# Optimization experiments

Hardware: AMD Instinct MI355X
Metric: run time of the kernel (lower is better)

Reference implementation:

```python
import jax, jax.numpy as jnp
import numpy as np

EOS_COEF = 0.1


def setup_inputs() -> dict:
    key = jax.random.key(0)
    k1, k2, k3, k4 = jax.random.split(key, 4)
    B, Q, T, P, M = 8, 256, 128, 100, 512
    pred_patch_logits = jax.random.normal(k1, (B, Q, 2), dtype=jnp.float32)
    pred_patch_points = jax.random.normal(k2, (B, Q, P, 3), dtype=jnp.float32)
    tgt_points = jax.random.normal(k3, (B, T, M, 3), dtype=jnp.float32)
    src_idx = jax.random.randint(k4, (B, T), 0, Q, dtype=jnp.int64)
    return {
        'pred_patch_logits': pred_patch_logits,
        'pred_patch_points': pred_patch_points,
        'tgt_points': tgt_points,
        'src_idx': src_idx,
    }


def reference(pred_patch_logits, pred_patch_points, tgt_points, src_idx):
    B, Q, C = pred_patch_logits.shape
    T = src_idx.shape[1]
    P = pred_patch_points.shape[2]
    M = tgt_points.shape[2]
    N = B * T  # total matched patches = num_patches
    bidx = jnp.arange(B)[:, None]

    # ---- loss_valid_labels (weighted CE, empty_weight = [1, eos_coef]) ----
    w = jnp.array([1.0, EOS_COEF], dtype=pred_patch_logits.dtype)
    target_classes = jnp.ones((B, Q), jnp.int32).at[bidx, src_idx].set(0)
    logp = jax.nn.log_softmax(pred_patch_logits, axis=-1)          # [B,Q,2]
    nll = -jnp.take_along_axis(logp, target_classes[..., None], axis=-1)[..., 0]
    wt = w[target_classes]
    loss_ce = jnp.sum(nll * wt) / jnp.sum(wt)

    # accuracy@1 on matched queries (targets are all class 0) and overall
    matched_logits = pred_patch_logits[bidx, src_idx]              # [B,T,2]
    acc_valid = 100.0 * jnp.mean((jnp.argmax(matched_logits, -1) == 0).astype(jnp.float32))
    acc_overall = 100.0 * jnp.mean((jnp.argmax(pred_patch_logits, -1) == target_classes).astype(jnp.float32))

    # ---- loss_cardinality (no-grad, logging) ----
    card_pred = jnp.sum((jnp.argmax(pred_patch_logits, -1) != (C - 1)).astype(jnp.float32), axis=1)
    card_err = jnp.mean(jnp.abs(card_pred - jnp.float32(T)))

    # ---- loss_geometry: per-patch squared chamfer, fused over all patches ----
    src = pred_patch_points[bidx, src_idx].reshape(N, P, 3)        # matched preds
    tgt = tgt_points.reshape(N, M, 3)
    # squared pairwise distances [N,P,M] = |a|^2 + |b|^2 - 2 a.b
    d2 = (jnp.sum(src * src, -1)[:, :, None]
          + jnp.sum(tgt * tgt, -1)[:, None, :]
          - 2.0 * jnp.einsum('npd,nmd->npm', src, tgt))
    d2 = jnp.maximum(d2, 0.0)
    per_patch = (jnp.mean(jnp.min(d2, axis=1), axis=-1)
                 + 0.2 * jnp.mean(jnp.min(d2, axis=2), axis=-1)) / 1.2  # [N]
    loss_geometry = jnp.sum(per_patch) / jnp.float32(N)

    return (loss_ce, acc_valid, acc_overall, card_err, loss_geometry)
```

## Files before the change

kernel.cpp:

```cpp
#include <hip/hip_runtime.h>
#include <math.h>

#define Bq 8
#define Qq 256
#define Tt 128
#define Pp 100
#define Mm 512
#define Nn 1024

__device__ __forceinline__ float breduce256(float v, float* red) {
    #pragma unroll
    for (int off = 32; off > 0; off >>= 1) v += __shfl_down(v, off, 64);
    __syncthreads();
    if ((threadIdx.x & 63) == 0) red[threadIdx.x >> 6] = v;
    __syncthreads();
    return red[0] + red[1] + red[2] + red[3];
}

__global__ __launch_bounds__(256) void geom_kernel(
    const float* __restrict__ pred_pts,
    const float* __restrict__ tgt_pts,
    const int*   __restrict__ src_idx,
    float*       __restrict__ per_patch)
{
    __shared__ float4   s_tgt[Mm];
    __shared__ float4   s_src[128];
    __shared__ unsigned s_amin[Mm];
    __shared__ float    s_bpart[8][128];
    __shared__ float    red[4];
    const int n   = blockIdx.x;
    const int tid = threadIdx.x;
    const int b   = n >> 7;
    const int q   = src_idx[n];
    const float* sp = pred_pts + (size_t)(b * Qq + q) * (Pp * 3);
    const float* tp = tgt_pts  + (size_t)n * (Mm * 3);

    {
        const float2* tp2 = (const float2*)tp;
        const float2 a = tp2[3*tid], c2 = tp2[3*tid+1], e = tp2[3*tid+2];
        s_tgt[2*tid]   = make_float4(a.x, a.y, c2.x, 0.f);
        s_tgt[2*tid+1] = make_float4(c2.y, e.x, e.y, 0.f);
    }
    if (tid < 50) {
        const float2* sp2 = (const float2*)sp;
        const float2 a = sp2[3*tid], c2 = sp2[3*tid+1], e = sp2[3*tid+2];
        s_src[2*tid]   = make_float4(a.x, a.y, c2.x, 0.f);
        s_src[2*tid+1] = make_float4(c2.y, e.x, e.y, 0.f);
    } else if (tid >= 100 && tid < 128) {
        s_src[tid] = make_float4(5e18f, 5e18f, 5e18f, 0.f);
    }
    *(uint2*)&s_amin[2*tid] = make_uint2(0x7f7fffffu, 0x7f7fffffu);
    __syncthreads();

    const int g = tid & 31;
    const int c = tid >> 5;
    const int mbase = c << 6;
    const float4 s0 = s_src[4*g+0], s1 = s_src[4*g+1],
                 s2 = s_src[4*g+2], s3 = s_src[4*g+3];
    float mn0 = 3.4e38f, mn1 = 3.4e38f, mn2 = 3.4e38f, mn3 = 3.4e38f;

    #pragma unroll 4
    for (int j = 0; j < 64; ++j) {
        const int m = mbase + ((j + g) & 63);
        const float4 t = s_tgt[m];
        float dx, dy, dz;
        dx = s0.x - t.x; dy = s0.y - t.y; dz = s0.z - t.z;
        const float d0 = fmaf(dx, dx, fmaf(dy, dy, dz * dz));
        dx = s1.x - t.x; dy = s1.y - t.y; dz = s1.z - t.z;
        const float d1 = fmaf(dx, dx, fmaf(dy, dy, dz * dz));
        dx = s2.x - t.x; dy = s2.y - t.y; dz = s2.z - t.z;
        const float d2 = fmaf(dx, dx, fmaf(dy, dy, dz * dz));
        dx = s3.x - t.x; dy = s3.y - t.y; dz = s3.z - t.z;
        const float d3 = fmaf(dx, dx, fmaf(dy, dy, dz * dz));
        mn0 = fminf(mn0, d0); mn1 = fminf(mn1, d1);
        mn2 = fminf(mn2, d2); mn3 = fminf(mn3, d3);
        const float pm = fminf(fminf(d0, d1), fminf(d2, d3));
        atomicMin(&s_amin[m], __float_as_uint(pm));
    }

    *(float4*)&s_bpart[c][4*g] = make_float4(mn0, mn1, mn2, mn3);
    __syncthreads();

    float contrib;
    {
        const uint2 u = *(const uint2*)&s_amin[2*tid];
        contrib = (__uint_as_float(u.x) + __uint_as_float(u.y)) * (1.0f / Mm);
    }
    if (tid < Pp) {
        float mn = s_bpart[0][tid];
        #pragma unroll
        for (int cc = 1; cc < 8; ++cc) mn = fminf(mn, s_bpart[cc][tid]);
        contrib += 0.2f * mn * (1.0f / Pp);
    }

    const float tot = breduce256(contrib, red);
    if (tid == 0) per_patch[n] = tot * (1.0f / 1.2f);
}

__global__ __launch_bounds__(256) void cls_kernel(
    const float* __restrict__ logits,
    const int*   __restrict__ src_idx,
    const float* __restrict__ per_patch,
    float*       __restrict__ out)
{
    __shared__ unsigned char matched[Bq * Qq];
    __shared__ int s_card[Bq];
    __shared__ float red[4];
    const int tid = threadIdx.x;
    for (int i = tid; i < Bq * Qq; i += 256) matched[i] = 0;
    if (tid < Bq) s_card[tid] = 0;
    __syncthreads();
    for (int i = tid; i < Nn; i += 256) {
        const int b = i >> 7;
        matched[b * Qq + src_idx[i]] = 1;
    }
    __syncthreads();

    float sum_nll = 0.f, sum_wt = 0.f, cnt_overall = 0.f;
    #pragma unroll
    for (int k = 0; k < (Bq * Qq) / 256; ++k) {
        const int i = tid + k * 256;
        const float l0 = logits[2*i], l1 = logits[2*i + 1];
        const int   mt = matched[i];
        const float mx  = fmaxf(l0, l1);
        const float lse = mx + logf(expf(l0 - mx) + expf(l1 - mx));
        const float lt  = mt ? l0 : l1;
        const float wt  = mt ? 1.0f : 0.1f;
        sum_nll += wt * (lse - lt);
        sum_wt  += wt;
        const int pred = (l0 >= l1) ? 0 : 1;
        const int c    = mt ? 0 : 1;
        cnt_overall += (pred == c) ? 1.f : 0.f;
        const unsigned long long bal = __ballot(pred == 0);
        if ((tid & 63) == 0) atomicAdd(&s_card[k], (int)__popcll(bal));
    }

    float cnt_valid = 0.f;
    for (int i = tid; i < Nn; i += 256) {
        const int b = i >> 7;
        const int q = src_idx[i];
        const float l0 = logits[2*(b*Qq + q)], l1 = logits[2*(b*Qq + q) + 1];
        cnt_valid += (l0 >= l1) ? 1.f : 0.f;
    }

    float gsum = 0.f;
    for (int i = tid; i < Nn; i += 256) gsum += per_patch[i];

    const float t_nll = breduce256(sum_nll,     red);
    const float t_wt  = breduce256(sum_wt,      red);
    const float t_ov  = breduce256(cnt_overall, red);
    const float t_va  = breduce256(cnt_valid,   red);
    const float t_gs  = breduce256(gsum,        red);
    __syncthreads();

    if (tid == 0) {
        float cerr = 0.f;
        for (int b = 0; b < Bq; ++b) cerr += fabsf((float)s_card[b] - (float)Tt);
        out[0] = t_nll / t_wt;
        out[1] = 100.f * t_va / (float)Nn;
        out[2] = 100.f * t_ov / (float)(Bq * Qq);
        out[3] = cerr / (float)Bq;
        out[4] = t_gs / (float)Nn;
    }
}

extern "C" void kernel_launch(void* const* d_in, const int* in_sizes, int n_in,
                              void* d_out, int out_size, void* d_ws, size_t ws_size,
                              hipStream_t stream) {
    const float* logits   = (const float*)d_in[0];
    const float* pred_pts = (const float*)d_in[1];
    const float* tgt_pts  = (const float*)d_in[2];
    const int*   src_idx  = (const int*)  d_in[3];
    float* out       = (float*)d_out;
    float* per_patch = (float*)d_ws;

    geom_kernel<<<Nn, 256, 0, stream>>>(pred_pts, tgt_pts, src_idx, per_patch);
    cls_kernel<<<1, 256, 0, stream>>>(logits, src_idx, per_patch, out);
}
```

Before: 86.73 us.

## Fuse classification into geometry kernel via last-block pattern and retile chamfer loop

Merges the single-block classification kernel into the geometry kernel. The last block to finish, found with an atomic done counter, computes the CE, accuracy, cardinality and final geometry sum, which removes a second launch but adds a memset per call. The chamfer inner loop is retiled so each thread holds 16 source points in registers against 16 targets, cutting target LDS reads and atomicMin count per distance. The target LDS layout is swizzled with an XOR to avoid bank conflicts. Per-source minima are now reduced with shared atomics instead of a partial array, and register pressure rises from holding 16 float4 plus 16 minima.

```diff
diff --git a/kernel.cpp b/kernel.cpp
--- a/kernel.cpp
+++ b/kernel.cpp
@@ -17,17 +17,21 @@
     return red[0] + red[1] + red[2] + red[3];
 }
 
-__global__ __launch_bounds__(256) void geom_kernel(
+__global__ __launch_bounds__(256) void fused_kernel(
+    const float* __restrict__ logits,
     const float* __restrict__ pred_pts,
     const float* __restrict__ tgt_pts,
     const int*   __restrict__ src_idx,
-    float*       __restrict__ per_patch)
+    float*       __restrict__ per_patch,
+    unsigned*    __restrict__ done_ctr,
+    float*       __restrict__ out)
 {
     __shared__ float4   s_tgt[Mm];
     __shared__ float4   s_src[128];
     __shared__ unsigned s_amin[Mm];
-    __shared__ float    s_bpart[8][128];
+    __shared__ unsigned s_bmin[128];
     __shared__ float    red[4];
+    __shared__ unsigned s_lastflag;
     const int n   = blockIdx.x;
     const int tid = threadIdx.x;
     const int b   = n >> 7;
@@ -38,8 +42,11 @@
     {
         const float2* tp2 = (const float2*)tp;
         const float2 a = tp2[3*tid], c2 = tp2[3*tid+1], e = tp2[3*tid+2];
-        s_tgt[2*tid]   = make_float4(a.x, a.y, c2.x, 0.f);
-        s_tgt[2*tid+1] = make_float4(c2.y, e.x, e.y, 0.f);
+        const int m0 = 2*tid, m1 = 2*tid + 1;
+        const int p0 = (m0 & ~15) | ((m0 & 15) ^ ((m0 >> 4) & 7));
+        const int p1 = (m1 & ~15) | ((m1 & 15) ^ ((m1 >> 4) & 7));
+        s_tgt[p0] = make_float4(a.x, a.y, c2.x, 0.f);
+        s_tgt[p1] = make_float4(c2.y, e.x, e.y, 0.f);
     }
     if (tid < 50) {
         const float2* sp2 = (const float2*)sp;
@@ -50,35 +57,43 @@
         s_src[tid] = make_float4(5e18f, 5e18f, 5e18f, 0.f);
     }
     *(uint2*)&s_amin[2*tid] = make_uint2(0x7f7fffffu, 0x7f7fffffu);
+    if (tid < 128) s_bmin[tid] = 0x7f7fffffu;
     __syncthreads();
 
-    const int g = tid & 31;
-    const int c = tid >> 5;
-    const int mbase = c << 6;
-    const float4 s0 = s_src[4*g+0], s1 = s_src[4*g+1],
-                 s2 = s_src[4*g+2], s3 = s_src[4*g+3];
-    float mn0 = 3.4e38f, mn1 = 3.4e38f, mn2 = 3.4e38f, mn3 = 3.4e38f;
+    const int g     = tid & 7;
+    const int c     = tid >> 3;
+    const int mswz  = c & 7;
+    const int mbase = c << 4;
+    float4 S[16];
+    #pragma unroll
+    for (int k = 0; k < 16; ++k) S[k] = s_src[16*g + k];
+    float mn[16];
+    #pragma unroll
+    for (int k = 0; k < 16; ++k) mn[k] = 3.4e38f;
 
-    #pragma unroll 4
-    for (int j = 0; j < 64; ++j) {
-        const int m = mbase + ((j + g) & 63);
-        const float4 t = s_tgt[m];
-        float dx, dy, dz;
-        dx = s0.x - t.x; dy = s0.y - t.y; dz = s0.z - t.z;
-        const float d0 = fmaf(dx, dx, fmaf(dy, dy, dz * dz));
-        dx = s1.x - t.x; dy = s1.y - t.y; dz = s1.z - t.z;
-        const float d1 = fmaf(dx, dx, fmaf(dy, dy, dz * dz));
-        dx = s2.x - t.x; dy = s2.y - t.y; dz = s2.z - t.z;
-        const float d2 = fmaf(dx, dx, fmaf(dy, dy, dz * dz));
-        dx = s3.x - t.x; dy = s3.y - t.y; dz = s3.z - t.z;
-        const float d3 = fmaf(dx, dx, fmaf(dy, dy, dz * dz));
-        mn0 = fminf(mn0, d0); mn1 = fminf(mn1, d1);
-        mn2 = fminf(mn2, d2); mn3 = fminf(mn3, d3);
-        const float pm = fminf(fminf(d0, d1), fminf(d2, d3));
-        atomicMin(&s_amin[m], __float_as_uint(pm));
+    #pragma unroll
+    for (int j = 0; j < 16; ++j) {
+        const int idx = mbase + (((j + g) & 15) ^ mswz);
+        const float4 t = s_tgt[idx];
+        float pmA = 3.4e38f, pmB = 3.4e38f, pmC = 3.4e38f, pmD = 3.4e38f;
+        #pragma unroll
+        for (int k = 0; k < 16; k += 4) {
+            float dx, dy, dz, d;
+            dx = S[k].x-t.x;   dy = S[k].y-t.y;   dz = S[k].z-t.z;
+            d = fmaf(dx,dx,fmaf(dy,dy,dz*dz)); mn[k]   = fminf(mn[k],   d); pmA = fminf(pmA, d);
+            dx = S[k+1].x-t.x; dy = S[k+1].y-t.y; dz = S[k+1].z-t.z;
+            d = fmaf(dx,dx,fmaf(dy,dy,dz*dz)); mn[k+1] = fminf(mn[k+1], d); pmB = fminf(pmB, d);
+            dx = S[k+2].x-t.x; dy = S[k+2].y-t.y; dz = S[k+2].z-t.z;
+            d = fmaf(dx,dx,fmaf(dy,dy,dz*dz)); mn[k+2] = fminf(mn[k+2], d); pmC = fminf(pmC, d);
+            dx = S[k+3].x-t.x; dy = S[k+3].y-t.y; dz = S[k+3].z-t.z;
+            d = fmaf(dx,dx,fmaf(dy,dy,dz*dz)); mn[k+3] = fminf(mn[k+3], d); pmD = fminf(pmD, d);
+        }
+        const float pm = fminf(fminf(pmA, pmB), fminf(pmC, pmD));
+        atomicMin(&s_amin[idx], __float_as_uint(pm));
     }
-
-    *(float4*)&s_bpart[c][4*g] = make_float4(mn0, mn1, mn2, mn3);
+    #pragma unroll
+    for (int k = 0; k < 16; ++k)
+        atomicMin(&s_bmin[16*g + k], __float_as_uint(mn[k]));
     __syncthreads();
 
     float contrib;
@@ -86,76 +101,57 @@
         const uint2 u = *(const uint2*)&s_amin[2*tid];
         contrib = (__uint_as_float(u.x) + __uint_as_float(u.y)) * (1.0f / Mm);
     }
-    if (tid < Pp) {
-        float mn = s_bpart[0][tid];
-        #pragma unroll
-        for (int cc = 1; cc < 8; ++cc) mn = fminf(mn, s_bpart[cc][tid]);
-        contrib += 0.2f * mn * (1.0f / Pp);
-    }
+    if (tid < Pp) contrib += 0.2f * __uint_as_float(s_bmin[tid]) * (1.0f / Pp);
 
     const float tot = breduce256(contrib, red);
-    if (tid == 0) per_patch[n] = tot * (1.0f / 1.2f);
-}
+    if (tid == 0) {
+        per_patch[n] = tot * (1.0f / 1.2f);
+        __threadfence();
+        s_lastflag = (atomicAdd(done_ctr, 1u) == (unsigned)(Nn - 1));
+    }
+    __syncthreads();
+    if (!s_lastflag) return;
 
-__global__ __launch_bounds__(256) void cls_kernel(
-    const float* __restrict__ logits,
-    const int*   __restrict__ src_idx,
-    const float* __restrict__ per_patch,
-    float*       __restrict__ out)
-{
     __shared__ unsigned char matched[Bq * Qq];
     __shared__ int s_card[Bq];
-    __shared__ float red[4];
-    const int tid = threadIdx.x;
     for (int i = tid; i < Bq * Qq; i += 256) matched[i] = 0;
     if (tid < Bq) s_card[tid] = 0;
     __syncthreads();
-    for (int i = tid; i < Nn; i += 256) {
-        const int b = i >> 7;
-        matched[b * Qq + src_idx[i]] = 1;
-    }
+    for (int i = tid; i < Nn; i += 256) matched[(i >> 7) * Qq + src_idx[i]] = 1;
     __syncthreads();
 
-    float sum_nll = 0.f, sum_wt = 0.f, cnt_overall = 0.f;
+    float sum_nll = 0.f, sum_wt = 0.f, cnt_ov = 0.f;
     #pragma unroll
-    for (int k = 0; k < (Bq * Qq) / 256; ++k) {
-        const int i = tid + k * 256;
-        const float l0 = logits[2*i], l1 = logits[2*i + 1];
-        const int   mt = matched[i];
-        const float mx  = fmaxf(l0, l1);
-        const float lse = mx + logf(expf(l0 - mx) + expf(l1 - mx));
-        const float lt  = mt ? l0 : l1;
-        const float wt  = mt ? 1.0f : 0.1f;
-        sum_nll += wt * (lse - lt);
-        sum_wt  += wt;
-        const int pred = (l0 >= l1) ? 0 : 1;
-        const int c    = mt ? 0 : 1;
-        cnt_overall += (pred == c) ? 1.f : 0.f;
-        const unsigned long long bal = __ballot(pred == 0);
+    for (int k = 0; k < 8; ++k) {
+        const int i = tid + (k << 8);
+        const float2 l = ((const float2*)logits)[i];
+        const int mt = matched[i];
+        const float mx  = fmaxf(l.x, l.y);
+        const float lse = mx + logf(expf(l.x - mx) + expf(l.y - mx));
+        sum_nll += (mt ? 1.0f : 0.1f) * (lse - (mt ? l.x : l.y));
+        sum_wt  += mt ? 1.0f : 0.1f;
+        const int pred0 = (l.x >= l.y) ? 1 : 0;
+        cnt_ov += (pred0 == mt) ? 1.f : 0.f;
+        const unsigned long long bal = __ballot(pred0);
         if ((tid & 63) == 0) atomicAdd(&s_card[k], (int)__popcll(bal));
     }
-
-    float cnt_valid = 0.f;
+    float cnt_va = 0.f, gsum = 0.f;
+    const volatile float* vpp = per_patch;
     for (int i = tid; i < Nn; i += 256) {
-        const int b = i >> 7;
-        const int q = src_idx[i];
-        const float l0 = logits[2*(b*Qq + q)], l1 = logits[2*(b*Qq + q) + 1];
-        cnt_valid += (l0 >= l1) ? 1.f : 0.f;
+        const float2 l = ((const float2*)logits)[(i >> 7) * Qq + src_idx[i]];
+        cnt_va += (l.x >= l.y) ? 1.f : 0.f;
+        gsum   += vpp[i];
     }
 
-    float gsum = 0.f;
-    for (int i = tid; i < Nn; i += 256) gsum += per_patch[i];
-
-    const float t_nll = breduce256(sum_nll,     red);
-    const float t_wt  = breduce256(sum_wt,      red);
-    const float t_ov  = breduce256(cnt_overall, red);
-    const float t_va  = breduce256(cnt_valid,   red);
-    const float t_gs  = breduce256(gsum,        red);
-    __syncthreads();
+    const float t_nll = breduce256(sum_nll, red);
+    const float t_wt  = breduce256(sum_wt,  red);
+    const float t_ov  = breduce256(cnt_ov,  red);
+    const float t_va  = breduce256(cnt_va,  red);
+    const float t_gs  = breduce256(gsum,    red);
 
     if (tid == 0) {
         float cerr = 0.f;
-        for (int b = 0; b < Bq; ++b) cerr += fabsf((float)s_card[b] - (float)Tt);
+        for (int bb = 0; bb < Bq; ++bb) cerr += fabsf((float)s_card[bb] - (float)Tt);
         out[0] = t_nll / t_wt;
         out[1] = 100.f * t_va / (float)Nn;
         out[2] = 100.f * t_ov / (float)(Bq * Qq);
@@ -173,7 +169,9 @@
     const int*   src_idx  = (const int*)  d_in[3];
     float* out       = (float*)d_out;
     float* per_patch = (float*)d_ws;
+    unsigned* ctr    = (unsigned*)((char*)d_ws + 4096);
 
-    geom_kernel<<<Nn, 256, 0, stream>>>(pred_pts, tgt_pts, src_idx, per_patch);
-    cls_kernel<<<1, 256, 0, stream>>>(logits, src_idx, per_patch, out);
+    hipMemsetAsync(ctr, 0, sizeof(unsigned), stream);
+    fused_kernel<<<Nn, 256, 0, stream>>>(logits, pred_pts, tgt_pts, src_idx,
+                                         per_patch, ctr, out);
 }
```

After: 103.9 us. 19.7% more time.
